# Optimization experiments

Hardware: AMD Instinct MI355X
Metric: run time of the kernel (lower is better)

Reference implementation:

```python
import jax, jax.numpy as jnp
import numpy as np

H = 8          # n_heads
M = 16         # max_dist
U = 512        # n_units
DH = U // H    # d_head
EPS = 1e-3     # keras LayerNormalization default epsilon
NEG = -2.0**32 + 1.0


def _rel_table(pe, T):
    # pe: [2M+1, DH]; returns [T, T, DH] with rel[i, j] = pe[clip(j - i, -M, M) + M]
    i = jnp.arange(T)
    idx = jnp.clip(i[None, :] - i[:, None], -M, M) + M
    return pe[idx]


def _split_heads(x):
    # [B, T, U] -> [H*B, T, DH]  (head-major, matching tf.concat(tf.split(x, H, 2), 0))
    B, T, _ = x.shape
    return x.reshape(B, T, H, DH).transpose(2, 0, 1, 3).reshape(H * B, T, DH)


def _merge_heads(x, B):
    # [H*B, T, DH] -> [B, T, U]
    T = x.shape[1]
    return x.reshape(H, B, T, DH).transpose(1, 2, 0, 3).reshape(B, T, U)


def setup_inputs() -> dict:
    key = jax.random.key(0)
    ks = jax.random.split(key, 10)
    B, T = 8, 1024
    s = 1.0 / np.sqrt(U)
    inp = {
        'q': jax.random.normal(ks[0], (B, T, U), jnp.float32),
        'k': jax.random.normal(ks[1], (B, T, U), jnp.float32),
        'v': jax.random.normal(ks[2], (B, T, U), jnp.float32),
        'Wq': jax.random.normal(ks[3], (U, U), jnp.float32) * s,
        'bq': jnp.zeros((U,), jnp.float32),
        'Wk': jax.random.normal(ks[4], (U, U), jnp.float32) * s,
        'bk': jnp.zeros((U,), jnp.float32),
        'Wv': jax.random.normal(ks[5], (U, U), jnp.float32) * s,
        'bv': jnp.zeros((U,), jnp.float32),
        'Wo': jax.random.normal(ks[6], (U, U), jnp.float32) * s,
        'bo': jnp.zeros((U,), jnp.float32),
        'gamma': jnp.ones((U,), jnp.float32),
        'beta': jnp.zeros((U,), jnp.float32),
        'pe_k': jax.random.normal(ks[7], (2 * M + 1, DH), jnp.float32) * 0.05,
        'pe_v': jax.random.normal(ks[8], (2 * M + 1, DH), jnp.float32) * 0.05,
    }
    return inp


def reference(q, k, v, Wq, bq, Wk, bk, Wv, bv, Wo, bo, gamma, beta, pe_k, pe_v):
    B, T, _ = q.shape
    relu = jax.nn.relu
    q_emb = relu(q @ Wq + bq)
    k_emb = relu(k @ Wk + bk)
    v_emb = relu(v @ Wv + bv)
    qh = _split_heads(q_emb)   # [HB, T, DH]
    kh = _split_heads(k_emb)
    vh = _split_heads(v_emb)

    attn = jnp.einsum('btd,bsd->bts', qh, kh)
    rel_k = _rel_table(pe_k, T)                       # [T, T, DH]
    attn = attn + jnp.einsum('btd,tsd->bts', qh, rel_k)
    attn = attn / jnp.asarray(DH, attn.dtype) ** 0.5

    causal = jnp.tril(jnp.ones((T, T), jnp.bool_))
    attn = jnp.where(causal[None], attn, jnp.asarray(NEG, attn.dtype))
    w = jax.nn.softmax(attn, axis=-1)

    out = jnp.einsum('bts,bsd->btd', w, vh)
    rel_v = _rel_table(pe_v, T)
    out = out + jnp.einsum('bts,tsd->btd', w, rel_v)

    out = _merge_heads(out, B)                        # [B, T, U]
    out = relu(out @ Wo + bo)
    out = out + q

    mu = jnp.mean(out, axis=-1, keepdims=True)
    var = jnp.mean(jnp.square(out - mu), axis=-1, keepdims=True)
    return (out - mu) * jax.lax.rsqrt(var + EPS) * gamma + beta
```

## Files before the change

### kernel.cpp

```cpp
#include <hip/hip_runtime.h>
#include <hip/hip_bf16.h>

#define T_SEQ 1024
#define U_DIM 512
#define LN_EPS 1e-3f

typedef float  f32x4  __attribute__((ext_vector_type(4)));
typedef short  bf16x8 __attribute__((ext_vector_type(8)));

__device__ __forceinline__ unsigned short f2bf(float f) {
    union { float f; unsigned u; } x; x.f = f;
    unsigned r = x.u + 0x7fffu + ((x.u >> 16) & 1u);
    return (unsigned short)(r >> 16);
}
__device__ __forceinline__ float b2f(short s) {
    union { unsigned u; float f; } x; x.u = ((unsigned)(unsigned short)s) << 16;
    return x.f;
}
__device__ __forceinline__ int packbf(float a, float b) {
    return (int)((unsigned)f2bf(a) | ((unsigned)f2bf(b) << 16));
}
__device__ __forceinline__ void async_copy16(void* lds, const void* g) {
    __builtin_amdgcn_global_load_lds((const __attribute__((address_space(1))) void*)g,
                                     (__attribute__((address_space(3))) void*)lds, 16, 0, 0);
}

__global__ __launch_bounds__(256) void prep_all(
        const float* __restrict__ Wq, const float* __restrict__ Wk,
        const float* __restrict__ Wv, const float* __restrict__ Wo,
        short* __restrict__ wt,
        const float* __restrict__ q, const float* __restrict__ k,
        const float* __restrict__ v,
        short* __restrict__ qb, short* __restrict__ kb, short* __restrict__ vb) {
    __shared__ float Ws[64][65];
    const int bid = blockIdx.x, t = threadIdx.x;
    if (bid < 256) {
        const int z = bid >> 6, tile = bid & 63;
        const float* W = (z == 0) ? Wq : (z == 1) ? Wk : (z == 2) ? Wv : Wo;
        short* Wt = wt + (size_t)z * 262144;
        const int k0 = (tile >> 3) * 64, n0 = (tile & 7) * 64;
        {
            const int kr = t >> 2, cs = (t & 3) * 16;
            const float4* src = (const float4*)(W + (size_t)(k0 + kr) * 512 + n0 + cs);
#pragma unroll
            for (int i = 0; i < 4; ++i) {
                float4 vv = src[i];
                Ws[kr][cs + 4 * i + 0] = vv.x;
                Ws[kr][cs + 4 * i + 1] = vv.y;
                Ws[kr][cs + 4 * i + 2] = vv.z;
                Ws[kr][cs + 4 * i + 3] = vv.w;
            }
        }
        __syncthreads();
        {
            const int nr = t >> 2, ks = (t & 3) * 16;
            int4 w0, w1;
            w0.x = packbf(Ws[ks + 0][nr], Ws[ks + 1][nr]);
            w0.y = packbf(Ws[ks + 2][nr], Ws[ks + 3][nr]);
            w0.z = packbf(Ws[ks + 4][nr], Ws[ks + 5][nr]);
            w0.w = packbf(Ws[ks + 6][nr], Ws[ks + 7][nr]);
            w1.x = packbf(Ws[ks + 8][nr], Ws[ks + 9][nr]);
            w1.y = packbf(Ws[ks + 10][nr], Ws[ks + 11][nr]);
            w1.z = packbf(Ws[ks + 12][nr], Ws[ks + 13][nr]);
            w1.w = packbf(Ws[ks + 14][nr], Ws[ks + 15][nr]);
            short* dst = Wt + (size_t)(n0 + nr) * 512 + k0 + ks;
            *(int4*)dst = w0;
            *(int4*)(dst + 8) = w1;
        }
    } else {
        const int aid = bid - 256;
        const int tsr = aid >> 10, chunk = aid & 1023;
        const float* src = ((tsr == 0) ? q : (tsr == 1) ? k : v) + (size_t)chunk * 4096 + t * 16;
        short* dst = ((tsr == 0) ? qb : (tsr == 1) ? kb : vb) + (size_t)chunk * 4096 + t * 16;
        float4 f0 = ((const float4*)src)[0];
        float4 f1 = ((const float4*)src)[1];
        float4 f2 = ((const float4*)src)[2];
        float4 f3 = ((const float4*)src)[3];
        int4 o0, o1;
        o0.x = packbf(f0.x, f0.y); o0.y = packbf(f0.z, f0.w);
        o0.z = packbf(f1.x, f1.y); o0.w = packbf(f1.z, f1.w);
        o1.x = packbf(f2.x, f2.y); o1.y = packbf(f2.z, f2.w);
        o1.z = packbf(f3.x, f3.y); o1.w = packbf(f3.z, f3.w);
        *(int4*)dst = o0;
        *(int4*)(dst + 8) = o1;
    }
}

template <int OUT>
__global__ __launch_bounds__(256) void gemm_bf16(
        const short* __restrict__ A0, const short* __restrict__ A1, const short* __restrict__ A2,
        const short* __restrict__ Wt0, const short* __restrict__ Wt1, const short* __restrict__ Wt2,
        const float* __restrict__ b0p, const float* __restrict__ b1p, const float* __restrict__ b2p,
        const float* __restrict__ resid,
        void* __restrict__ O0, void* __restrict__ O1, void* __restrict__ O2) {
    __shared__ short As[2 * 8192];
    __shared__ short Bs[2 * 8192];

    const int z = blockIdx.z;
    const short* Az = (z == 0) ? A0 : (z == 1) ? A1 : A2;
    const short* Wz = (z == 0) ? Wt0 : (z == 1) ? Wt1 : Wt2;
    const float* bz = (z == 0) ? b0p : (z == 1) ? b1p : b2p;
    void* Ov = (z == 0) ? O0 : (z == 1) ? O1 : O2;

    const int tid = threadIdx.x;
    const int m0 = blockIdx.x * 128, n0 = blockIdx.y * 128;
    const int w = tid >> 6, lane = tid & 63;
    const int n15 = lane & 15, g = lane >> 4;
    const int mh = w >> 1, nh = w & 1;

    f32x4 acc[4][4];
#pragma unroll
    for (int i = 0; i < 4; ++i)
#pragma unroll
        for (int j = 0; j < 4; ++j) acc[i][j] = (f32x4){0.f, 0.f, 0.f, 0.f};

#define GEMM_STAGE(CK, BUF)                                                              \
    do {                                                                                 \
        const int k0s = (CK) * 64;                                                       \
        short* Ab = As + (BUF) * 8192;                                                   \
        short* Bb = Bs + (BUF) * 8192;                                                   \
        if (w < 2) {                                                                     \
            _Pragma("unroll")                                                            \
            for (int i = 0; i < 8; ++i) {                                                \
                const int kc = i >> 2, nt = w * 4 + (i & 3);                             \
                const short* gp = Wz + (size_t)(n0 + nt * 16 + n15) * 512 + k0s + kc * 32 + g * 8; \
                async_copy16(Bb + (kc * 8 + nt) * 512, gp);                              \
            }                                                                            \
        } else {                                                                         \
            _Pragma("unroll")                                                            \
            for (int i = 0; i < 8; ++i) {                                                \
                const int kc = i >> 2, mt = (w - 2) * 4 + (i & 3);                       \
                const short* gp = Az + (size_t)(m0 + mt * 16 + n15) * 512 + k0s + kc * 32 + g * 8; \
                async_copy16(Ab + (kc * 8 + mt) * 512, gp);                              \
            }                                                                            \
        }                                                                                \
    } while (0)

    GEMM_STAGE(0, 0);
    for (int ck = 0; ck < 8; ++ck) {
        __syncthreads();
        if (ck < 7) GEMM_STAGE(ck + 1, (ck + 1) & 1);
        const int buf = ck & 1;
#pragma unroll
        for (int kc = 0; kc < 2; ++kc) {
            bf16x8 af[4], bfv[4];
#pragma unroll
            for (int i = 0; i < 4; ++i)
                af[i] = *(const bf16x8*)(As + buf * 8192 + (kc * 8 + mh * 4 + i) * 512 + lane * 8);
#pragma unroll
            for (int j = 0; j < 4; ++j)
                bfv[j] = *(const bf16x8*)(Bs + buf * 8192 + (kc * 8 + nh * 4 + j) * 512 + lane * 8);
#pragma unroll
            for (int i = 0; i < 4; ++i)
#pragma unroll
                for (int j = 0; j < 4; ++j)
                    acc[i][j] = __builtin_amdgcn_mfma_f32_16x16x32_bf16(af[i], bfv[j], acc[i][j], 0, 0, 0);
        }
    }
#undef GEMM_STAGE

    const int mbase = m0 + mh * 64 + g * 4;
    const int nbase = n0 + nh * 64 + n15;
    const bool even = (n15 & 1) == 0;
    float bj[4];
#pragma unroll
    for (int j = 0; j < 4; ++j) bj[j] = bz[nbase + j * 16];

#pragma unroll
    for (int i = 0; i < 4; ++i) {
        const int mrow = mbase + i * 16;
#pragma unroll
        for (int j = 0; j < 4; ++j) {
            const int ncol = nbase + j * 16;
            f32x4 a = acc[i][j];
            float v0 = fmaxf(a[0] + bj[j], 0.f);
            float v1 = fmaxf(a[1] + bj[j], 0.f);
            float v2 = fmaxf(a[2] + bj[j], 0.f);
            float v3 = fmaxf(a[3] + bj[j], 0.f);
            if (OUT == 0) {
                unsigned t01 = (unsigned)packbf(v0, v1);
                unsigned t23 = (unsigned)packbf(v2, v3);
                unsigned x01 = (unsigned)__shfl_xor((int)t01, 1, 64);
                unsigned x23 = (unsigned)__shfl_xor((int)t23, 1, 64);
                short* Oz = (short*)Ov;
                if (even) {
                    unsigned d0 = (t01 & 0xffffu) | (x01 << 16);
                    unsigned d1 = (t01 >> 16) | (x01 & 0xffff0000u);
                    *(unsigned*)(Oz + (size_t)(mrow + 0) * 512 + ncol) = d0;
                    *(unsigned*)(Oz + (size_t)(mrow + 1) * 512 + ncol) = d1;
                } else {
                    unsigned d2 = (x23 & 0xffffu) | (t23 << 16);
                    unsigned d3 = (x23 >> 16) | (t23 & 0xffff0000u);
                    *(unsigned*)(Oz + (size_t)(mrow + 2) * 512 + ncol - 1) = d2;
                    *(unsigned*)(Oz + (size_t)(mrow + 3) * 512 + ncol - 1) = d3;
                }
            } else {
                float x0 = __shfl_xor(v0, 1, 64);
                float x1 = __shfl_xor(v1, 1, 64);
                float x2 = __shfl_xor(v2, 1, 64);
                float x3 = __shfl_xor(v3, 1, 64);
                float* Oz = (float*)Ov;
                if (even) {
                    float2 r0 = *(const float2*)(resid + (size_t)(mrow + 0) * 512 + ncol);
                    float2 r1 = *(const float2*)(resid + (size_t)(mrow + 1) * 512 + ncol);
                    *(float2*)(Oz + (size_t)(mrow + 0) * 512 + ncol) = make_float2(v0 + r0.x, x0 + r0.y);
                    *(float2*)(Oz + (size_t)(mrow + 1) * 512 + ncol) = make_float2(v1 + r1.x, x1 + r1.y);
                } else {
                    float2 r2 = *(const float2*)(resid + (size_t)(mrow + 2) * 512 + ncol - 1);
                    float2 r3 = *(const float2*)(resid + (size_t)(mrow + 3) * 512 + ncol - 1);
                    *(float2*)(Oz + (size_t)(mrow + 2) * 512 + ncol - 1) = make_float2(x2 + r2.x, v2 + r2.y);
                    *(float2*)(Oz + (size_t)(mrow + 3) * 512 + ncol - 1) = make_float2(x3 + r3.x, v3 + r3.y);
                }
            }
        }
    }
}

__global__ __launch_bounds__(256) void attn_mfma(
        const short* __restrict__ qe, const short* __restrict__ ke,
        const short* __restrict__ ve, const float* __restrict__ pe_k,
        float* __restrict__ ml, short* __restrict__ ao) {
    __shared__ short Kc[2 * 4096];
    __shared__ short Vt[2 * 4608];
    __shared__ float qpeS[4 * 32 * 17];

    const int tid = threadIdx.x;
    const int qt = 7 - (int)blockIdx.x;
    const int hb = blockIdx.y;
    const int h = hb >> 3, b = hb & 7;
    const int t0 = qt * 128;
    const int w = tid >> 6, lane = tid & 63;
    const int g = lane >> 4, n15 = lane & 15;
    const int qn[2] = {t0 + w * 16, t0 + (7 - w) * 16};
    const int wqhi = qn[1] + 15;
    const int nsteps = (t0 + 128) >> 6;
    const int sp = tid & 31, dbase = (tid >> 5) * 8;

    float* qpeW = qpeS + w * (32 * 17);

    bf16x8 Bq[2][2];
#pragma unroll
    for (int nt = 0; nt < 2; ++nt)
#pragma unroll
    for (int kh = 0; kh < 2; ++kh)
        Bq[nt][kh] = *(const bf16x8*)(qe + (size_t)(b * T_SEQ + qn[nt] + n15) * U_DIM
                                      + h * 64 + kh * 32 + g * 8);

    {
        f32x4 qa[2][2];
#pragma unroll
        for (int mt = 0; mt < 2; ++mt)
#pragma unroll
        for (int nt = 0; nt < 2; ++nt) qa[mt][nt] = (f32x4){0.f, 0.f, 0.f, 0.f};
#pragma unroll
        for (int mt = 0; mt < 2; ++mt)
#pragma unroll
        for (int kh = 0; kh < 2; ++kh) {
            const float* src = pe_k + (mt * 16 + n15) * 64 + kh * 32 + g * 8;
            float4 f0 = *(const float4*)src;
            float4 f1 = *(const float4*)(src + 4);
            bf16x8 fr;
            fr[0] = (short)f2bf(f0.x); fr[1] = (short)f2bf(f0.y);
            fr[2] = (short)f2bf(f0.z); fr[3] = (short)f2bf(f0.w);
            fr[4] = (short)f2bf(f1.x); fr[5] = (short)f2bf(f1.y);
            fr[6] = (short)f2bf(f1.z); fr[7] = (short)f2bf(f1.w);
#pragma unroll
            for (int nt = 0; nt < 2; ++nt)
                qa[mt][nt] = __builtin_amdgcn_mfma_f32_16x16x32_bf16(fr, Bq[nt][kh], qa[mt][nt], 0, 0, 0);
        }
#pragma unroll
        for (int mt = 0; mt < 2; ++mt)
#pragma unroll
        for (int nt = 0; nt < 2; ++nt)
#pragma unroll
        for (int r = 0; r < 4; ++r) {
            const int ri = mt * 16 + 4 * g + r;
            if (ri <= 16) qpeW[(nt * 16 + n15) * 17 + ri] = qa[mt][nt][r];
        }
    }
    const float qpe0r[2] = { qpeW[(n15) * 17], qpeW[(16 + n15) * 17] };

    float m_r[2] = {-3.0e38f, -3.0e38f};
    float l_r[2] = {0.f, 0.f};
    f32x4 oacc[2][4];
#pragma unroll
    for (int nt = 0; nt < 2; ++nt)
#pragma unroll
    for (int dt = 0; dt < 4; ++dt) oacc[nt][dt] = (f32x4){0.f, 0.f, 0.f, 0.f};

    {
#pragma unroll
        for (int j = 0; j < 2; ++j) {
            const int cc = 2 * w + j, kh = cc >> 2, mt = cc & 3;
            const short* gp = ke + (size_t)(b * T_SEQ + mt * 16 + n15) * U_DIM + h * 64 + kh * 32 + g * 8;
            async_copy16(Kc + cc * 512, gp);
        }
        const short* r0 = ve + (size_t)(b * T_SEQ + 2 * sp) * U_DIM + h * 64 + dbase;
        bf16x8 vx = *(const bf16x8*)r0, vy = *(const bf16x8*)(r0 + U_DIM);
#pragma unroll
        for (int ii = 0; ii < 8; ++ii) {
            int pv = (int)((unsigned short)vx[ii]) | (((int)(unsigned short)vy[ii]) << 16);
            *(int*)(Vt + (dbase + ii) * 72 + 2 * sp) = pv;
        }
    }

    for (int i = 0; i < nsteps; ++i) {
        const int s0 = i << 6;
        const int cbuf = i & 1, nbuf = cbuf ^ 1;
        const bool hasnext = (i + 1) < nsteps;
        bf16x8 vx, vy;
        __syncthreads();
        if (hasnext) {
            const int sn = s0 + 64;
#pragma unroll
            for (int j = 0; j < 2; ++j) {
                const int cc = 2 * w + j, kh = cc >> 2, mt = cc & 3;
                const short* gp = ke + (size_t)(b * T_SEQ + sn + mt * 16 + n15) * U_DIM + h * 64 + kh * 32 + g * 8;
                async_copy16(Kc + nbuf * 4096 + cc * 512, gp);
            }
            const short* r0 = ve + (size_t)(b * T_SEQ + sn + 2 * sp) * U_DIM + h * 64 + dbase;
            vx = *(const bf16x8*)r0;
            vy = *(const bf16x8*)(r0 + U_DIM);
        }

        if (s0 <= wqhi) {
            int cls[4][2];
#pragma unroll
            for (int mt = 0; mt < 4; ++mt)
#pragma unroll
            for (int nt = 0; nt < 2; ++nt) {
                const int slo = s0 + mt * 16;
                const int qlo = qn[nt];
                cls[mt][nt] = (slo > qlo + 15) ? 0 : ((slo + 31 < qlo) ? 1 : 2);
            }

            f32x4 c[4][2];
#pragma unroll
            for (int mt = 0; mt < 4; ++mt)
#pragma unroll
            for (int nt = 0; nt < 2; ++nt) c[mt][nt] = (f32x4){0.f, 0.f, 0.f, 0.f};
#pragma unroll
            for (int mt = 0; mt < 4; ++mt) {
                if (cls[mt][0] == 0 && cls[mt][1] == 0) continue;
#pragma unroll
                for (int kh = 0; kh < 2; ++kh) {
                    bf16x8 ak = *(const bf16x8*)(Kc + cbuf * 4096 + (kh * 4 + mt) * 512 + lane * 8);
#pragma unroll
                    for (int nt = 0; nt < 2; ++nt)
                        if (cls[mt][nt])
                            c[mt][nt] = __builtin_amdgcn_mfma_f32_16x16x32_bf16(ak, Bq[nt][kh], c[mt][nt], 0, 0, 0);
                }
            }

            float p[4][2][4];
            float alpha_l[2];
#pragma unroll
            for (int nt = 0; nt < 2; ++nt) {
                const int qg = qn[nt] + n15;
                float sc[4][4];
                float pmax = -3.0e38f;
#pragma unroll
                for (int mt = 0; mt < 4; ++mt) {
                    if (cls[mt][nt] == 0) {
#pragma unroll
                        for (int r = 0; r < 4; ++r) sc[mt][r] = -3.0e38f;
                    } else if (cls[mt][nt] == 1) {
#pragma unroll
                        for (int r = 0; r < 4; ++r) {
                            sc[mt][r] = (c[mt][nt][r] + qpe0r[nt]) * 0.125f;
                            pmax = fmaxf(pmax, sc[mt][r]);
                        }
                    } else {
#pragma unroll
                        for (int r = 0; r < 4; ++r) {
                            const int sg = s0 + mt * 16 + 4 * g + r;
                            const int dlt = sg - qg;
                            if (dlt <= 0) {
                                const int ri = (dlt < -16) ? 0 : (dlt + 16);
                                sc[mt][r] = (c[mt][nt][r] + qpeW[(nt * 16 + n15) * 17 + ri]) * 0.125f;
                                pmax = fmaxf(pmax, sc[mt][r]);
                            } else {
                                sc[mt][r] = -3.0e38f;
                            }
                        }
                    }
                }
                pmax = fmaxf(pmax, __shfl_xor(pmax, 16, 64));
                pmax = fmaxf(pmax, __shfl_xor(pmax, 32, 64));
                const float mnew = fmaxf(m_r[nt], pmax);
                const float alpha = __expf(m_r[nt] - mnew);
                float psum = 0.f;
#pragma unroll
                for (int mt = 0; mt < 4; ++mt)
#pragma unroll
                for (int r = 0; r < 4; ++r) {
                    const float pv = (cls[mt][nt] == 0) ? 0.f : __expf(sc[mt][r] - mnew);
                    p[mt][nt][r] = pv;
                    psum += pv;
                }
                psum += __shfl_xor(psum, 16, 64);
                psum += __shfl_xor(psum, 32, 64);
                l_r[nt] = l_r[nt] * alpha + psum;
                m_r[nt] = mnew;
                alpha_l[nt] = alpha;
            }

            int pk01[4][2], pk23[4][2];
#pragma unroll
            for (int mt = 0; mt < 4; ++mt)
#pragma unroll
            for (int nt = 0; nt < 2; ++nt) {
                pk01[mt][nt] = packbf(p[mt][nt][0], p[mt][nt][1]);
                pk23[mt][nt] = packbf(p[mt][nt][2], p[mt][nt][3]);
            }
            const int srcA = ((g & 1) * 2) * 16 + n15;
            const int srcB = srcA + 16;
            const bool selHi = (g >> 1) != 0;
#pragma unroll
            for (int nt = 0; nt < 2; ++nt) {
                float aO[4];
#pragma unroll
                for (int r = 0; r < 4; ++r) aO[r] = __shfl(alpha_l[nt], 4 * g + r, 64);
#pragma unroll
                for (int dt = 0; dt < 4; ++dt)
#pragma unroll
                for (int r = 0; r < 4; ++r) oacc[nt][dt][r] *= aO[r];
#pragma unroll
                for (int kh = 0; kh < 2; ++kh) {
                    if (cls[2 * kh][nt] == 0 && cls[2 * kh + 1][nt] == 0) continue;
                    const int a0l = __shfl(pk01[2 * kh][nt], srcA, 64);
                    const int a0h = __shfl(pk01[2 * kh + 1][nt], srcA, 64);
                    const int a1l = __shfl(pk23[2 * kh][nt], srcA, 64);
                    const int a1h = __shfl(pk23[2 * kh + 1][nt], srcA, 64);
                    const int a2l = __shfl(pk01[2 * kh][nt], srcB, 64);
                    const int a2h = __shfl(pk01[2 * kh + 1][nt], srcB, 64);
                    const int a3l = __shfl(pk23[2 * kh][nt], srcB, 64);
                    const int a3h = __shfl(pk23[2 * kh + 1][nt], srcB, 64);
                    union { int i[4]; bf16x8 v; } au;
                    au.i[0] = selHi ? a0h : a0l;
                    au.i[1] = selHi ? a1h : a1l;
                    au.i[2] = selHi ? a2h : a2l;
                    au.i[3] = selHi ? a3h : a3l;
#pragma unroll
                    for (int dt = 0; dt < 4; ++dt) {
                        bf16x8 bv = *(const bf16x8*)(Vt + cbuf * 4608 + (dt * 16 + n15) * 72 + kh * 32 + g * 8);
                        oacc[nt][dt] = __builtin_amdgcn_mfma_f32_16x16x32_bf16(au.v, bv, oacc[nt][dt], 0, 0, 0);
                    }
                }
            }
        }

        if (hasnext) {
#pragma unroll
            for (int ii = 0; ii < 8; ++ii) {
                int pv = (int)((unsigned short)vx[ii]) | (((int)(unsigned short)vy[ii]) << 16);
                *(int*)(Vt + nbuf * 4608 + (dbase + ii) * 72 + 2 * sp) = pv;
            }
        }
    }

#pragma unroll
    for (int nt = 0; nt < 2; ++nt) {
        if (g == 0) {
            float2 v2 = make_float2(m_r[nt], l_r[nt]);
            *(float2*)(ml + ((size_t)hb * T_SEQ + qn[nt] + n15) * 2) = v2;
        }
    }
#pragma unroll
    for (int nt = 0; nt < 2; ++nt)
#pragma unroll
    for (int r = 0; r < 4; ++r) {
        const float lq = __shfl(l_r[nt], 4 * g + r, 64);
        const float linv = 1.0f / lq;
        const int qg = qn[nt] + 4 * g + r;
        short* dst = ao + (size_t)(b * T_SEQ + qg) * U_DIM + h * 64 + n15;
#pragma unroll
        for (int dt = 0; dt < 4; ++dt)
            dst[dt * 16] = (short)f2bf(oacc[nt][dt][r] * linv);
    }
}

__global__ __launch_bounds__(256) void band_relv(
        const short* __restrict__ qe, const short* __restrict__ ke,
        const float* __restrict__ pe_k, const float* __restrict__ pe_v,
        const float* __restrict__ ml, short* __restrict__ ao) {
    __shared__ float pek[17 * 64];
    __shared__ float pev[17 * 64];
    const int tb = blockIdx.x, hb = blockIdx.y;
    const int h = hb >> 3, b = hb & 7;
    const int tid = threadIdx.x;
    for (int i = tid; i < 17 * 64; i += 256) {
        pek[i] = b2f((short)f2bf(pe_k[i]));
        pev[i] = pe_v[i];
    }
    __syncthreads();

    const int t = tb * 64 + (tid >> 2);
    const int p = (tid & 3) * 16;
    const short* qp = qe + (size_t)(b * T_SEQ + t) * U_DIM + h * 64 + p;
    bf16x8 qa = *(const bf16x8*)qp, qb2 = *(const bf16x8*)(qp + 8);
    float qv[16];
#pragma unroll
    for (int i = 0; i < 8; ++i) { qv[i] = b2f(qa[i]); qv[8 + i] = b2f(qb2[i]); }

    float dots[17];
#pragma unroll
    for (int ri = 0; ri < 17; ++ri) {
        const int s = t - 16 + ri;
        float acc = 0.f;
        if (s >= 0) {
            const short* kp = ke + (size_t)(b * T_SEQ + s) * U_DIM + h * 64 + p;
            bf16x8 ka = *(const bf16x8*)kp, kb2 = *(const bf16x8*)(kp + 8);
#pragma unroll
            for (int d = 0; d < 8; ++d) {
                acc += qv[d] * b2f(ka[d]);
                acc += qv[8 + d] * b2f(kb2[d]);
            }
#pragma unroll
            for (int d = 0; d < 16; ++d) acc += qv[d] * pek[ri * 64 + p + d];
        }
        dots[ri] = acc;
    }
#pragma unroll
    for (int ri = 0; ri < 17; ++ri) {
        dots[ri] += __shfl_xor(dots[ri], 1, 64);
        dots[ri] += __shfl_xor(dots[ri], 2, 64);
    }

    const float2 mlv = *(const float2*)(ml + ((size_t)hb * T_SEQ + t) * 2);
    const float m = mlv.x, linv = 1.0f / mlv.y;
    float wv[17];
    float wsum = 0.f;
#pragma unroll
    for (int ri = 0; ri < 17; ++ri) {
        const int s = t - 16 + ri;
        const float wr = (s >= 0) ? __expf(dots[ri] * 0.125f - m) * linv : 0.f;
        wv[ri] = wr;
        wsum += wr;
    }
    wv[0] += 1.0f - wsum;

    float relv[16];
#pragma unroll
    for (int d = 0; d < 16; ++d) relv[d] = 0.f;
#pragma unroll
    for (int ri = 0; ri < 17; ++ri)
#pragma unroll
        for (int d = 0; d < 16; ++d) relv[d] += wv[ri] * pev[ri * 64 + p + d];

    short* op = ao + (size_t)(b * T_SEQ + t) * U_DIM + h * 64 + p;
    bf16x8 a0 = *(const bf16x8*)op, a1 = *(const bf16x8*)(op + 8);
    int4 o0, o1;
    o0.x = packbf(b2f(a0[0]) + relv[0],  b2f(a0[1]) + relv[1]);
    o0.y = packbf(b2f(a0[2]) + relv[2],  b2f(a0[3]) + relv[3]);
    o0.z = packbf(b2f(a0[4]) + relv[4],  b2f(a0[5]) + relv[5]);
    o0.w = packbf(b2f(a0[6]) + relv[6],  b2f(a0[7]) + relv[7]);
    o1.x = packbf(b2f(a1[0]) + relv[8],  b2f(a1[1]) + relv[9]);
    o1.y = packbf(b2f(a1[2]) + relv[10], b2f(a1[3]) + relv[11]);
    o1.z = packbf(b2f(a1[4]) + relv[12], b2f(a1[5]) + relv[13]);
    o1.w = packbf(b2f(a1[6]) + relv[14], b2f(a1[7]) + relv[15]);
    *(int4*)op = o0;
    *(int4*)(op + 8) = o1;
}

__global__ __launch_bounds__(256) void ln_kernel(float* __restrict__ io,
                                                 const float* __restrict__ gamma,
                                                 const float* __restrict__ beta) {
    const int row = blockIdx.x * 4 + (threadIdx.x >> 6);
    const int lane = threadIdx.x & 63;
    float* rp = io + (size_t)row * 512 + lane * 8;
    float4 a = *(const float4*)rp;
    float4 c = *(const float4*)(rp + 4);
    float v[8] = {a.x, a.y, a.z, a.w, c.x, c.y, c.z, c.w};

    float s = v[0] + v[1] + v[2] + v[3] + v[4] + v[5] + v[6] + v[7];
#pragma unroll
    for (int off = 1; off < 64; off <<= 1) s += __shfl_xor(s, off, 64);
    const float mu = s * (1.0f / 512.0f);

    float sq = 0.f;
#pragma unroll
    for (int i = 0; i < 8; ++i) { v[i] -= mu; sq += v[i] * v[i]; }
#pragma unroll
    for (int off = 1; off < 64; off <<= 1) sq += __shfl_xor(sq, off, 64);
    const float rs = rsqrtf(sq * (1.0f / 512.0f) + LN_EPS);

    const float4 g0 = *(const float4*)(gamma + lane * 8);
    const float4 g1 = *(const float4*)(gamma + lane * 8 + 4);
    const float4 b0 = *(const float4*)(beta + lane * 8);
    const float4 b1 = *(const float4*)(beta + lane * 8 + 4);
    float4 o0, o1;
    o0.x = v[0] * rs * g0.x + b0.x;
    o0.y = v[1] * rs * g0.y + b0.y;
    o0.z = v[2] * rs * g0.z + b0.z;
    o0.w = v[3] * rs * g0.w + b0.w;
    o1.x = v[4] * rs * g1.x + b1.x;
    o1.y = v[5] * rs * g1.y + b1.y;
    o1.z = v[6] * rs * g1.z + b1.z;
    o1.w = v[7] * rs * g1.w + b1.w;
    *(float4*)rp = o0;
    *(float4*)(rp + 4) = o1;
}

extern "C" void kernel_launch(void* const* d_in, const int* in_sizes, int n_in,
                              void* d_out, int out_size, void* d_ws, size_t ws_size,
                              hipStream_t stream) {
    const float* q     = (const float*)d_in[0];
    const float* k     = (const float*)d_in[1];
    const float* v     = (const float*)d_in[2];
    const float* Wq    = (const float*)d_in[3];
    const float* bq    = (const float*)d_in[4];
    const float* Wk    = (const float*)d_in[5];
    const float* bk    = (const float*)d_in[6];
    const float* Wv    = (const float*)d_in[7];
    const float* bv    = (const float*)d_in[8];
    const float* Wo    = (const float*)d_in[9];
    const float* bo    = (const float*)d_in[10];
    const float* gamma = (const float*)d_in[11];
    const float* beta  = (const float*)d_in[12];
    const float* pe_k  = (const float*)d_in[13];
    const float* pe_v  = (const float*)d_in[14];
    float* out = (float*)d_out;

    char* base = (char*)d_ws;
    short* qb = (short*)(base);
    short* kb = (short*)(base + (((size_t)8) << 20));
    short* vb = (short*)(base + (((size_t)16) << 20));
    short* qe = (short*)(base + (((size_t)24) << 20));
    short* ke = (short*)(base + (((size_t)32) << 20));
    short* ve = (short*)(base + (((size_t)40) << 20));
    short* ao = (short*)(base + (((size_t)48) << 20));
    short* wt = (short*)(base + (((size_t)56) << 20));
    float* ml = (float*)(base + (((size_t)58) << 20));
    short* wtq = wt, *wtk = wt + 262144, *wtv = wt + 2 * 262144, *wto = wt + 3 * 262144;

    prep_all<<<dim3(3328), 256, 0, stream>>>(Wq, Wk, Wv, Wo, wt, q, k, v, qb, kb, vb);
    gemm_bf16<0><<<dim3(64, 4, 3), 256, 0, stream>>>(
        qb, kb, vb, wtq, wtk, wtv, bq, bk, bv, nullptr, qe, ke, ve);
    attn_mfma<<<dim3(8, 64), 256, 0, stream>>>(qe, ke, ve, pe_k, ml, ao);
    band_relv<<<dim3(16, 64), 256, 0, stream>>>(qe, ke, pe_k, pe_v, ml, ao);
    gemm_bf16<1><<<dim3(64, 4, 1), 256, 0, stream>>>(
        ao, ao, ao, wto, wto, wto, bo, bo, bo, q, out, out, out);
    ln_kernel<<<dim3(2048), 256, 0, stream>>>(out, gamma, beta);
}
```

Before: 273.1 us.

## Drop LDS staging in GEMM and attention, write V transposed from projection

The GEMM now loads MFMA fragments straight from global memory into registers, with one-step register prefetch, in place of double-buffered async copies to LDS. The V projection epilogue writes V directly in a per-head transposed [hb][d][s] layout, so the attention kernel reads K and V fragments from global memory without LDS staging or an in-kernel transpose. Attention is restructured so each wave handles one 16-row query tile over two balanced phases (tiles bx and 15-bx). This removes barriers and LDS traffic, but relies on L1/L2 caching for reuse across waves and adds global-load latency.

```diff
diff --git a/kernel.cpp b/kernel.cpp
--- a/kernel.cpp
+++ b/kernel.cpp
@@ -19,10 +19,6 @@
 }
 __device__ __forceinline__ int packbf(float a, float b) {
     return (int)((unsigned)f2bf(a) | ((unsigned)f2bf(b) << 16));
-}
-__device__ __forceinline__ void async_copy16(void* lds, const void* g) {
-    __builtin_amdgcn_global_load_lds((const __attribute__((address_space(1))) void*)g,
-                                     (__attribute__((address_space(3))) void*)lds, 16, 0, 0);
 }
 
 __global__ __launch_bounds__(256) void prep_all(
@@ -87,15 +83,12 @@
 }
 
 template <int OUT>
-__global__ __launch_bounds__(256) void gemm_bf16(
+__global__ __launch_bounds__(256) void gemm_nolds(
         const short* __restrict__ A0, const short* __restrict__ A1, const short* __restrict__ A2,
         const short* __restrict__ Wt0, const short* __restrict__ Wt1, const short* __restrict__ Wt2,
         const float* __restrict__ b0p, const float* __restrict__ b1p, const float* __restrict__ b2p,
         const float* __restrict__ resid,
         void* __restrict__ O0, void* __restrict__ O1, void* __restrict__ O2) {
-    __shared__ short As[2 * 8192];
-    __shared__ short Bs[2 * 8192];
-
     const int z = blockIdx.z;
     const short* Az = (z == 0) ? A0 : (z == 1) ? A1 : A2;
     const short* Wz = (z == 0) ? Wt0 : (z == 1) ? Wt1 : Wt2;
@@ -108,56 +101,42 @@
     const int n15 = lane & 15, g = lane >> 4;
     const int mh = w >> 1, nh = w & 1;
 
+    const short* Ab = Az + (size_t)(m0 + mh * 64 + n15) * 512 + g * 8;
+    const short* Bb = Wz + (size_t)(n0 + nh * 64 + n15) * 512 + g * 8;
+
     f32x4 acc[4][4];
 #pragma unroll
     for (int i = 0; i < 4; ++i)
 #pragma unroll
         for (int j = 0; j < 4; ++j) acc[i][j] = (f32x4){0.f, 0.f, 0.f, 0.f};
 
-#define GEMM_STAGE(CK, BUF)                                                              \
-    do {                                                                                 \
-        const int k0s = (CK) * 64;                                                       \
-        short* Ab = As + (BUF) * 8192;                                                   \
-        short* Bb = Bs + (BUF) * 8192;                                                   \
-        if (w < 2) {                                                                     \
-            _Pragma("unroll")                                                            \
-            for (int i = 0; i < 8; ++i) {                                                \
-                const int kc = i >> 2, nt = w * 4 + (i & 3);                             \
-                const short* gp = Wz + (size_t)(n0 + nt * 16 + n15) * 512 + k0s + kc * 32 + g * 8; \
-                async_copy16(Bb + (kc * 8 + nt) * 512, gp);                              \
-            }                                                                            \
-        } else {                                                                         \
-            _Pragma("unroll")                                                            \
-            for (int i = 0; i < 8; ++i) {                                                \
-                const int kc = i >> 2, mt = (w - 2) * 4 + (i & 3);                       \
-                const short* gp = Az + (size_t)(m0 + mt * 16 + n15) * 512 + k0s + kc * 32 + g * 8; \
-                async_copy16(Ab + (kc * 8 + mt) * 512, gp);                              \
-            }                                                                            \
-        }                                                                                \
-    } while (0)
-
-    GEMM_STAGE(0, 0);
-    for (int ck = 0; ck < 8; ++ck) {
-        __syncthreads();
-        if (ck < 7) GEMM_STAGE(ck + 1, (ck + 1) & 1);
-        const int buf = ck & 1;
-#pragma unroll
-        for (int kc = 0; kc < 2; ++kc) {
-            bf16x8 af[4], bfv[4];
-#pragma unroll
-            for (int i = 0; i < 4; ++i)
-                af[i] = *(const bf16x8*)(As + buf * 8192 + (kc * 8 + mh * 4 + i) * 512 + lane * 8);
+    bf16x8 af[4], bfv[4];
+#pragma unroll
+    for (int t = 0; t < 4; ++t) {
+        af[t]  = *(const bf16x8*)(Ab + t * 16 * 512);
+        bfv[t] = *(const bf16x8*)(Bb + t * 16 * 512);
+    }
+#pragma unroll
+    for (int kk = 0; kk < 16; ++kk) {
+        bf16x8 afn[4], bfn[4];
+        if (kk < 15) {
+            const int ko = (kk + 1) * 32;
+#pragma unroll
+            for (int t = 0; t < 4; ++t) {
+                afn[t] = *(const bf16x8*)(Ab + t * 16 * 512 + ko);
+                bfn[t] = *(const bf16x8*)(Bb + t * 16 * 512 + ko);
+            }
+        }
+#pragma unroll
+        for (int i = 0; i < 4; ++i)
 #pragma unroll
             for (int j = 0; j < 4; ++j)
-                bfv[j] = *(const bf16x8*)(Bs + buf * 8192 + (kc * 8 + nh * 4 + j) * 512 + lane * 8);
-#pragma unroll
-            for (int i = 0; i < 4; ++i)
-#pragma unroll
-                for (int j = 0; j < 4; ++j)
-                    acc[i][j] = __builtin_amdgcn_mfma_f32_16x16x32_bf16(af[i], bfv[j], acc[i][j], 0, 0, 0);
-        }
-    }
-#undef GEMM_STAGE
+                acc[i][j] = __builtin_amdgcn_mfma_f32_16x16x32_bf16(af[i], bfv[j], acc[i][j], 0, 0, 0);
+        if (kk < 15) {
+#pragma unroll
+            for (int t = 0; t < 4; ++t) { af[t] = afn[t]; bfv[t] = bfn[t]; }
+        }
+    }
 
     const int mbase = m0 + mh * 64 + g * 4;
     const int nbase = n0 + nh * 64 + n15;
@@ -165,6 +144,27 @@
     float bj[4];
 #pragma unroll
     for (int j = 0; j < 4; ++j) bj[j] = bz[nbase + j * 16];
+
+    if (OUT == 0 && z == 2) {
+        const int b = m0 >> 10;
+        const int sbase = (m0 & 1023) + mh * 64 + g * 4;
+        short* vTo = (short*)Ov;
+#pragma unroll
+        for (int i = 0; i < 4; ++i) {
+            const int srow = sbase + i * 16;
+#pragma unroll
+            for (int j = 0; j < 4; ++j) {
+                const int col = nbase + j * 16;
+                const int h = col >> 6, d = col & 63;
+                f32x4 a = acc[i][j];
+                int2 pv;
+                pv.x = packbf(fmaxf(a[0] + bj[j], 0.f), fmaxf(a[1] + bj[j], 0.f));
+                pv.y = packbf(fmaxf(a[2] + bj[j], 0.f), fmaxf(a[3] + bj[j], 0.f));
+                *(int2*)(vTo + (size_t)(h * 8 + b) * 65536 + d * 1024 + srow) = pv;
+            }
+        }
+        return;
+    }
 
 #pragma unroll
     for (int i = 0; i < 4; ++i) {
@@ -218,265 +218,186 @@
 
 __global__ __launch_bounds__(256) void attn_mfma(
         const short* __restrict__ qe, const short* __restrict__ ke,
-        const short* __restrict__ ve, const float* __restrict__ pe_k,
+        const short* __restrict__ vT, const float* __restrict__ pe_k,
         float* __restrict__ ml, short* __restrict__ ao) {
-    __shared__ short Kc[2 * 4096];
-    __shared__ short Vt[2 * 4608];
-    __shared__ float qpeS[4 * 32 * 17];
+    __shared__ float qpeS[4 * 16 * 17];
 
     const int tid = threadIdx.x;
-    const int qt = 7 - (int)blockIdx.x;
+    const int bx = blockIdx.x;
     const int hb = blockIdx.y;
     const int h = hb >> 3, b = hb & 7;
-    const int t0 = qt * 128;
     const int w = tid >> 6, lane = tid & 63;
     const int g = lane >> 4, n15 = lane & 15;
-    const int qn[2] = {t0 + w * 16, t0 + (7 - w) * 16};
-    const int wqhi = qn[1] + 15;
-    const int nsteps = (t0 + 128) >> 6;
-    const int sp = tid & 31, dbase = (tid >> 5) * 8;
-
-    float* qpeW = qpeS + w * (32 * 17);
-
-    bf16x8 Bq[2][2];
-#pragma unroll
-    for (int nt = 0; nt < 2; ++nt)
-#pragma unroll
-    for (int kh = 0; kh < 2; ++kh)
-        Bq[nt][kh] = *(const bf16x8*)(qe + (size_t)(b * T_SEQ + qn[nt] + n15) * U_DIM
-                                      + h * 64 + kh * 32 + g * 8);
-
-    {
-        f32x4 qa[2][2];
-#pragma unroll
-        for (int mt = 0; mt < 2; ++mt)
-#pragma unroll
-        for (int nt = 0; nt < 2; ++nt) qa[mt][nt] = (f32x4){0.f, 0.f, 0.f, 0.f};
-#pragma unroll
-        for (int mt = 0; mt < 2; ++mt)
-#pragma unroll
-        for (int kh = 0; kh < 2; ++kh) {
-            const float* src = pe_k + (mt * 16 + n15) * 64 + kh * 32 + g * 8;
-            float4 f0 = *(const float4*)src;
-            float4 f1 = *(const float4*)(src + 4);
-            bf16x8 fr;
-            fr[0] = (short)f2bf(f0.x); fr[1] = (short)f2bf(f0.y);
-            fr[2] = (short)f2bf(f0.z); fr[3] = (short)f2bf(f0.w);
-            fr[4] = (short)f2bf(f1.x); fr[5] = (short)f2bf(f1.y);
-            fr[6] = (short)f2bf(f1.z); fr[7] = (short)f2bf(f1.w);
-#pragma unroll
-            for (int nt = 0; nt < 2; ++nt)
-                qa[mt][nt] = __builtin_amdgcn_mfma_f32_16x16x32_bf16(fr, Bq[nt][kh], qa[mt][nt], 0, 0, 0);
-        }
-#pragma unroll
-        for (int mt = 0; mt < 2; ++mt)
-#pragma unroll
-        for (int nt = 0; nt < 2; ++nt)
-#pragma unroll
-        for (int r = 0; r < 4; ++r) {
-            const int ri = mt * 16 + 4 * g + r;
-            if (ri <= 16) qpeW[(nt * 16 + n15) * 17 + ri] = qa[mt][nt][r];
-        }
-    }
-    const float qpe0r[2] = { qpeW[(n15) * 17], qpeW[(16 + n15) * 17] };
-
-    float m_r[2] = {-3.0e38f, -3.0e38f};
-    float l_r[2] = {0.f, 0.f};
-    f32x4 oacc[2][4];
-#pragma unroll
-    for (int nt = 0; nt < 2; ++nt)
-#pragma unroll
-    for (int dt = 0; dt < 4; ++dt) oacc[nt][dt] = (f32x4){0.f, 0.f, 0.f, 0.f};
-
-    {
-#pragma unroll
-        for (int j = 0; j < 2; ++j) {
-            const int cc = 2 * w + j, kh = cc >> 2, mt = cc & 3;
-            const short* gp = ke + (size_t)(b * T_SEQ + mt * 16 + n15) * U_DIM + h * 64 + kh * 32 + g * 8;
-            async_copy16(Kc + cc * 512, gp);
-        }
-        const short* r0 = ve + (size_t)(b * T_SEQ + 2 * sp) * U_DIM + h * 64 + dbase;
-        bf16x8 vx = *(const bf16x8*)r0, vy = *(const bf16x8*)(r0 + U_DIM);
-#pragma unroll
-        for (int ii = 0; ii < 8; ++ii) {
-            int pv = (int)((unsigned short)vx[ii]) | (((int)(unsigned short)vy[ii]) << 16);
-            *(int*)(Vt + (dbase + ii) * 72 + 2 * sp) = pv;
-        }
-    }
-
-    for (int i = 0; i < nsteps; ++i) {
-        const int s0 = i << 6;
-        const int cbuf = i & 1, nbuf = cbuf ^ 1;
-        const bool hasnext = (i + 1) < nsteps;
-        bf16x8 vx, vy;
-        __syncthreads();
-        if (hasnext) {
-            const int sn = s0 + 64;
-#pragma unroll
-            for (int j = 0; j < 2; ++j) {
-                const int cc = 2 * w + j, kh = cc >> 2, mt = cc & 3;
-                const short* gp = ke + (size_t)(b * T_SEQ + sn + mt * 16 + n15) * U_DIM + h * 64 + kh * 32 + g * 8;
-                async_copy16(Kc + nbuf * 4096 + cc * 512, gp);
-            }
-            const short* r0 = ve + (size_t)(b * T_SEQ + sn + 2 * sp) * U_DIM + h * 64 + dbase;
-            vx = *(const bf16x8*)r0;
-            vy = *(const bf16x8*)(r0 + U_DIM);
-        }
-
-        if (s0 <= wqhi) {
-            int cls[4][2];
-#pragma unroll
-            for (int mt = 0; mt < 4; ++mt)
-#pragma unroll
-            for (int nt = 0; nt < 2; ++nt) {
+    float* qpeW = qpeS + w * (16 * 17);
+    const size_t rowbase = (size_t)b * T_SEQ;
+    const short* kbase = ke + (rowbase + n15) * 512 + h * 64 + g * 8;
+    const short* vbase = vT + (size_t)hb * 65536 + n15 * 1024 + g * 8;
+
+#pragma unroll 1
+    for (int ph = 0; ph < 2; ++ph) {
+        const int tile = (ph == 0) ? bx : 15 - bx;
+        const int qn = tile * 64 + w * 16;
+
+        bf16x8 Bq[2];
+#pragma unroll
+        for (int kh = 0; kh < 2; ++kh)
+            Bq[kh] = *(const bf16x8*)(qe + (rowbase + qn + n15) * U_DIM + h * 64 + kh * 32 + g * 8);
+
+        {
+            f32x4 qa[2];
+            qa[0] = (f32x4){0.f, 0.f, 0.f, 0.f};
+            qa[1] = (f32x4){0.f, 0.f, 0.f, 0.f};
+#pragma unroll
+            for (int mt = 0; mt < 2; ++mt)
+#pragma unroll
+            for (int kh = 0; kh < 2; ++kh) {
+                const float* src = pe_k + (mt * 16 + n15) * 64 + kh * 32 + g * 8;
+                float4 f0 = *(const float4*)src;
+                float4 f1 = *(const float4*)(src + 4);
+                bf16x8 fr;
+                fr[0] = (short)f2bf(f0.x); fr[1] = (short)f2bf(f0.y);
+                fr[2] = (short)f2bf(f0.z); fr[3] = (short)f2bf(f0.w);
+                fr[4] = (short)f2bf(f1.x); fr[5] = (short)f2bf(f1.y);
+                fr[6] = (short)f2bf(f1.z); fr[7] = (short)f2bf(f1.w);
+                qa[mt] = __builtin_amdgcn_mfma_f32_16x16x32_bf16(fr, Bq[kh], qa[mt], 0, 0, 0);
+            }
+#pragma unroll
+            for (int mt = 0; mt < 2; ++mt)
+#pragma unroll
+            for (int r = 0; r < 4; ++r) {
+                const int ri = mt * 16 + 4 * g + r;
+                if (ri <= 16) qpeW[n15 * 17 + ri] = qa[mt][r];
+            }
+        }
+        const float qpe0 = qpeW[n15 * 17];
+
+        float m_r = -3.0e38f, l_r = 0.f;
+        f32x4 oacc[4];
+#pragma unroll
+        for (int dt = 0; dt < 4; ++dt) oacc[dt] = (f32x4){0.f, 0.f, 0.f, 0.f};
+
+        const int qg = qn + n15;
+        for (int s0 = 0; s0 <= qn + 15; s0 += 64) {
+            int cls[4];
+#pragma unroll
+            for (int mt = 0; mt < 4; ++mt) {
                 const int slo = s0 + mt * 16;
-                const int qlo = qn[nt];
-                cls[mt][nt] = (slo > qlo + 15) ? 0 : ((slo + 31 < qlo) ? 1 : 2);
-            }
-
-            f32x4 c[4][2];
-#pragma unroll
-            for (int mt = 0; mt < 4; ++mt)
-#pragma unroll
-            for (int nt = 0; nt < 2; ++nt) c[mt][nt] = (f32x4){0.f, 0.f, 0.f, 0.f};
+                cls[mt] = (slo > qn + 15) ? 0 : ((slo + 31 < qn) ? 1 : 2);
+            }
+
+            f32x4 c[4];
+#pragma unroll
+            for (int mt = 0; mt < 4; ++mt) c[mt] = (f32x4){0.f, 0.f, 0.f, 0.f};
 #pragma unroll
             for (int mt = 0; mt < 4; ++mt) {
-                if (cls[mt][0] == 0 && cls[mt][1] == 0) continue;
+                if (!cls[mt]) continue;
+                const short* kp = kbase + (size_t)(s0 + mt * 16) * 512;
 #pragma unroll
                 for (int kh = 0; kh < 2; ++kh) {
-                    bf16x8 ak = *(const bf16x8*)(Kc + cbuf * 4096 + (kh * 4 + mt) * 512 + lane * 8);
-#pragma unroll
-                    for (int nt = 0; nt < 2; ++nt)
-                        if (cls[mt][nt])
-                            c[mt][nt] = __builtin_amdgcn_mfma_f32_16x16x32_bf16(ak, Bq[nt][kh], c[mt][nt], 0, 0, 0);
+                    bf16x8 ak = *(const bf16x8*)(kp + kh * 32);
+                    c[mt] = __builtin_amdgcn_mfma_f32_16x16x32_bf16(ak, Bq[kh], c[mt], 0, 0, 0);
                 }
             }
 
-            float p[4][2][4];
-            float alpha_l[2];
-#pragma unroll
-            for (int nt = 0; nt < 2; ++nt) {
-                const int qg = qn[nt] + n15;
-                float sc[4][4];
-                float pmax = -3.0e38f;
-#pragma unroll
-                for (int mt = 0; mt < 4; ++mt) {
-                    if (cls[mt][nt] == 0) {
-#pragma unroll
-                        for (int r = 0; r < 4; ++r) sc[mt][r] = -3.0e38f;
-                    } else if (cls[mt][nt] == 1) {
-#pragma unroll
-                        for (int r = 0; r < 4; ++r) {
-                            sc[mt][r] = (c[mt][nt][r] + qpe0r[nt]) * 0.125f;
+            float sc[4][4];
+            float pmax = -3.0e38f;
+#pragma unroll
+            for (int mt = 0; mt < 4; ++mt) {
+                if (cls[mt] == 0) {
+#pragma unroll
+                    for (int r = 0; r < 4; ++r) sc[mt][r] = -3.0e38f;
+                } else if (cls[mt] == 1) {
+#pragma unroll
+                    for (int r = 0; r < 4; ++r) {
+                        sc[mt][r] = (c[mt][r] + qpe0) * 0.125f;
+                        pmax = fmaxf(pmax, sc[mt][r]);
+                    }
+                } else {
+#pragma unroll
+                    for (int r = 0; r < 4; ++r) {
+                        const int sg = s0 + mt * 16 + 4 * g + r;
+                        const int dlt = sg - qg;
+                        if (dlt <= 0) {
+                            const int ri = (dlt < -16) ? 0 : (dlt + 16);
+                            sc[mt][r] = (c[mt][r] + qpeW[n15 * 17 + ri]) * 0.125f;
                             pmax = fmaxf(pmax, sc[mt][r]);
-                        }
-                    } else {
-#pragma unroll
-                        for (int r = 0; r < 4; ++r) {
-                            const int sg = s0 + mt * 16 + 4 * g + r;
-                            const int dlt = sg - qg;
-                            if (dlt <= 0) {
-                                const int ri = (dlt < -16) ? 0 : (dlt + 16);
-                                sc[mt][r] = (c[mt][nt][r] + qpeW[(nt * 16 + n15) * 17 + ri]) * 0.125f;
-                                pmax = fmaxf(pmax, sc[mt][r]);
-                            } else {
-                                sc[mt][r] = -3.0e38f;
-                            }
+                        } else {
+                            sc[mt][r] = -3.0e38f;
                         }
                     }
                 }
-                pmax = fmaxf(pmax, __shfl_xor(pmax, 16, 64));
-                pmax = fmaxf(pmax, __shfl_xor(pmax, 32, 64));
-                const float mnew = fmaxf(m_r[nt], pmax);
-                const float alpha = __expf(m_r[nt] - mnew);
-                float psum = 0.f;
-#pragma unroll
-                for (int mt = 0; mt < 4; ++mt)
-#pragma unroll
-                for (int r = 0; r < 4; ++r) {
-                    const float pv = (cls[mt][nt] == 0) ? 0.f : __expf(sc[mt][r] - mnew);
-                    p[mt][nt][r] = pv;
-                    psum += pv;
-                }
-                psum += __shfl_xor(psum, 16, 64);
-                psum += __shfl_xor(psum, 32, 64);
-                l_r[nt] = l_r[nt] * alpha + psum;
-                m_r[nt] = mnew;
-                alpha_l[nt] = alpha;
-            }
-
-            int pk01[4][2], pk23[4][2];
+            }
+            pmax = fmaxf(pmax, __shfl_xor(pmax, 16, 64));
+            pmax = fmaxf(pmax, __shfl_xor(pmax, 32, 64));
+            const float mnew = fmaxf(m_r, pmax);
+            const float alpha = __expf(m_r - mnew);
+            float p[4][4];
+            float psum = 0.f;
 #pragma unroll
             for (int mt = 0; mt < 4; ++mt)
 #pragma unroll
-            for (int nt = 0; nt < 2; ++nt) {
-                pk01[mt][nt] = packbf(p[mt][nt][0], p[mt][nt][1]);
-                pk23[mt][nt] = packbf(p[mt][nt][2], p[mt][nt][3]);
+            for (int r = 0; r < 4; ++r) {
+                const float pv = (cls[mt] == 0) ? 0.f : __expf(sc[mt][r] - mnew);
+                p[mt][r] = pv;
+                psum += pv;
+            }
+            psum += __shfl_xor(psum, 16, 64);
+            psum += __shfl_xor(psum, 32, 64);
+            l_r = l_r * alpha + psum;
+            m_r = mnew;
+
+            int pk01[4], pk23[4];
+#pragma unroll
+            for (int mt = 0; mt < 4; ++mt) {
+                pk01[mt] = packbf(p[mt][0], p[mt][1]);
+                pk23[mt] = packbf(p[mt][2], p[mt][3]);
             }
             const int srcA = ((g & 1) * 2) * 16 + n15;
             const int srcB = srcA + 16;
             const bool selHi = (g >> 1) != 0;
-#pragma unroll
-            for (int nt = 0; nt < 2; ++nt) {
-                float aO[4];
-#pragma unroll
-                for (int r = 0; r < 4; ++r) aO[r] = __shfl(alpha_l[nt], 4 * g + r, 64);
-#pragma unroll
-                for (int dt = 0; dt < 4; ++dt)
-#pragma unroll
-                for (int r = 0; r < 4; ++r) oacc[nt][dt][r] *= aO[r];
-#pragma unroll
-                for (int kh = 0; kh < 2; ++kh) {
-                    if (cls[2 * kh][nt] == 0 && cls[2 * kh + 1][nt] == 0) continue;
-                    const int a0l = __shfl(pk01[2 * kh][nt], srcA, 64);
-                    const int a0h = __shfl(pk01[2 * kh + 1][nt], srcA, 64);
-                    const int a1l = __shfl(pk23[2 * kh][nt], srcA, 64);
-                    const int a1h = __shfl(pk23[2 * kh + 1][nt], srcA, 64);
-                    const int a2l = __shfl(pk01[2 * kh][nt], srcB, 64);
-                    const int a2h = __shfl(pk01[2 * kh + 1][nt], srcB, 64);
-                    const int a3l = __shfl(pk23[2 * kh][nt], srcB, 64);
-                    const int a3h = __shfl(pk23[2 * kh + 1][nt], srcB, 64);
-                    union { int i[4]; bf16x8 v; } au;
-                    au.i[0] = selHi ? a0h : a0l;
-                    au.i[1] = selHi ? a1h : a1l;
-                    au.i[2] = selHi ? a2h : a2l;
-                    au.i[3] = selHi ? a3h : a3l;
-#pragma unroll
-                    for (int dt = 0; dt < 4; ++dt) {
-                        bf16x8 bv = *(const bf16x8*)(Vt + cbuf * 4608 + (dt * 16 + n15) * 72 + kh * 32 + g * 8);
-                        oacc[nt][dt] = __builtin_amdgcn_mfma_f32_16x16x32_bf16(au.v, bv, oacc[nt][dt], 0, 0, 0);
-                    }
+            float aO[4];
+#pragma unroll
+            for (int r = 0; r < 4; ++r) aO[r] = __shfl(alpha, 4 * g + r, 64);
+#pragma unroll
+            for (int dt = 0; dt < 4; ++dt)
+#pragma unroll
+            for (int r = 0; r < 4; ++r) oacc[dt][r] *= aO[r];
+#pragma unroll
+            for (int kh = 0; kh < 2; ++kh) {
+                if (cls[2 * kh] == 0 && cls[2 * kh + 1] == 0) continue;
+                const int a0l = __shfl(pk01[2 * kh], srcA, 64);
+                const int a0h = __shfl(pk01[2 * kh + 1], srcA, 64);
+                const int a1l = __shfl(pk23[2 * kh], srcA, 64);
+                const int a1h = __shfl(pk23[2 * kh + 1], srcA, 64);
+                const int a2l = __shfl(pk01[2 * kh], srcB, 64);
+                const int a2h = __shfl(pk01[2 * kh + 1], srcB, 64);
+                const int a3l = __shfl(pk23[2 * kh], srcB, 64);
+                const int a3h = __shfl(pk23[2 * kh + 1], srcB, 64);
+                union { int i[4]; bf16x8 v; } au;
+                au.i[0] = selHi ? a0h : a0l;
+                au.i[1] = selHi ? a1h : a1l;
+                au.i[2] = selHi ? a2h : a2l;
+                au.i[3] = selHi ? a3h : a3l;
+                const short* vp = vbase + s0 + kh * 32;
+#pragma unroll
+                for (int dt = 0; dt < 4; ++dt) {
+                    bf16x8 bv = *(const bf16x8*)(vp + dt * 16 * 1024);
+                    oacc[dt] = __builtin_amdgcn_mfma_f32_16x16x32_bf16(au.v, bv, oacc[dt], 0, 0, 0);
                 }
             }
         }
 
-        if (hasnext) {
-#pragma unroll
-            for (int ii = 0; ii < 8; ++ii) {
-                int pv = (int)((unsigned short)vx[ii]) | (((int)(unsigned short)vy[ii]) << 16);
-                *(int*)(Vt + nbuf * 4608 + (dbase + ii) * 72 + 2 * sp) = pv;
-            }
-        }
-    }
-
-#pragma unroll
-    for (int nt = 0; nt < 2; ++nt) {
-        if (g == 0) {
-            float2 v2 = make_float2(m_r[nt], l_r[nt]);
-            *(float2*)(ml + ((size_t)hb * T_SEQ + qn[nt] + n15) * 2) = v2;
-        }
-    }
-#pragma unroll
-    for (int nt = 0; nt < 2; ++nt)
-#pragma unroll
-    for (int r = 0; r < 4; ++r) {
-        const float lq = __shfl(l_r[nt], 4 * g + r, 64);
-        const float linv = 1.0f / lq;
-        const int qg = qn[nt] + 4 * g + r;
-        short* dst = ao + (size_t)(b * T_SEQ + qg) * U_DIM + h * 64 + n15;
-#pragma unroll
-        for (int dt = 0; dt < 4; ++dt)
-            dst[dt * 16] = (short)f2bf(oacc[nt][dt][r] * linv);
+        if (g == 0)
+            *(float2*)(ml + ((size_t)hb * T_SEQ + qn + n15) * 2) = make_float2(m_r, l_r);
+#pragma unroll
+        for (int r = 0; r < 4; ++r) {
+            const float lq = __shfl(l_r, 4 * g + r, 64);
+            const float linv = 1.0f / lq;
+            short* dst = ao + (rowbase + qn + 4 * g + r) * U_DIM + h * 64 + n15;
+#pragma unroll
+            for (int dt = 0; dt < 4; ++dt)
+                dst[dt * 16] = (short)f2bf(oacc[dt][r] * linv);
+        }
     }
 }
 
@@ -628,18 +549,18 @@
     short* vb = (short*)(base + (((size_t)16) << 20));
     short* qe = (short*)(base + (((size_t)24) << 20));
     short* ke = (short*)(base + (((size_t)32) << 20));
-    short* ve = (short*)(base + (((size_t)40) << 20));
+    short* vT = (short*)(base + (((size_t)40) << 20));
     short* ao = (short*)(base + (((size_t)48) << 20));
     short* wt = (short*)(base + (((size_t)56) << 20));
     float* ml = (float*)(base + (((size_t)58) << 20));
     short* wtq = wt, *wtk = wt + 262144, *wtv = wt + 2 * 262144, *wto = wt + 3 * 262144;
 
     prep_all<<<dim3(3328), 256, 0, stream>>>(Wq, Wk, Wv, Wo, wt, q, k, v, qb, kb, vb);
-    gemm_bf16<0><<<dim3(64, 4, 3), 256, 0, stream>>>(
-        qb, kb, vb, wtq, wtk, wtv, bq, bk, bv, nullptr, qe, ke, ve);
-    attn_mfma<<<dim3(8, 64), 256, 0, stream>>>(qe, ke, ve, pe_k, ml, ao);
+    gemm_nolds<0><<<dim3(64, 4, 3), 256, 0, stream>>>(
+        qb, kb, vb, wtq, wtk, wtv, bq, bk, bv, nullptr, qe, ke, vT);
+    attn_mfma<<<dim3(8, 64), 256, 0, stream>>>(qe, ke, vT, pe_k, ml, ao);
     band_relv<<<dim3(16, 64), 256, 0, stream>>>(qe, ke, pe_k, pe_v, ml, ao);
-    gemm_bf16<1><<<dim3(64, 4, 1), 256, 0, stream>>>(
+    gemm_nolds<1><<<dim3(64, 4, 1), 256, 0, stream>>>(
         ao, ao, ao, wto, wto, wto, bo, bo, bo, q, out, out, out);
     ln_kernel<<<dim3(2048), 256, 0, stream>>>(out, gamma, beta);
 }
```

Result: slower. 293.7 us (+7.6%).
